# Optimization experiments

Hardware: AMD Instinct MI355X
Metric: run time of the kernel (lower is better)

## Reference

```python
import jax, jax.numpy as jnp
import numpy as np

K_BINS, EMB_WIDTH = 2048, 64
N, T = 8, 8192

def setup_inputs() -> dict:
    key = jax.random.key(0)
    k1, k2 = jax.random.split(key)
    x = jax.random.normal(k1, (N, EMB_WIDTH, T), dtype=jnp.float32)
    mask = jnp.ones((N, 1, T), dtype=jnp.float32)
    k = jax.random.normal(k2, (K_BINS, EMB_WIDTH), dtype=jnp.float32)
    return {"x": x, "mask": mask, "k": k}

def reference(x, mask, k):
    # Faithful forward of BottleneckBlock.forward with update_k=False and
    # codebook `k` already initialized (init path is a stateful randperm init).
    n, c, t = x.shape
    w = k.shape[1]
    # preprocess: [N, W, T] -> [N*T, W]
    xf = jnp.transpose(x, (0, 2, 1)).reshape(-1, c)
    mf = jnp.transpose(mask, (0, 2, 1)).reshape(-1, 1)
    prenorm = jnp.linalg.norm(xf - jnp.mean(xf)) / np.sqrt(float(xf.size))
    dist = (jnp.sum(xf * xf, axis=-1, keepdims=True)
            - 2.0 * (xf @ k.T)
            + jnp.sum(k * k, axis=-1)[None, :])  # [N*T, k_bins]
    x_l = jnp.argmin(dist, axis=-1)              # [N*T]
    fit = jax.lax.stop_gradient(jnp.mean(jnp.min(dist, axis=-1)))
    x_d = jax.lax.stop_gradient(k[x_l])          # dequantize, no_grad in torch
    # commit loss: mask is 0/1, so masked-row norm^2 == sum(mask * diff^2)
    diff2 = jnp.sum((x_d - xf) ** 2, axis=-1, keepdims=True)
    commit_loss = jnp.sum(mf * diff2) / (jnp.sum(mf) * w)
    # straight-through estimator + mask
    x_d = (xf + jax.lax.stop_gradient(x_d - xf)) * mf
    # postprocess: back to [N, W, T] and [N, T]
    x_d = jnp.transpose(x_d.reshape(n, t, w), (0, 2, 1))
    x_l = x_l.reshape(n, t)
    return x_l, x_d, commit_loss, fit, prenorm
```

## Files before the change

kernel.cpp:

```cpp
#include <hip/hip_runtime.h>

#define T_DIM 8192
#define N_DIM 8
#define C_DIM 64
#define KB    2048
#define NT    (N_DIM * T_DIM)
#define TOTX  ((size_t)NT * C_DIM)
#define NBLK  2048
#define LISTCAP 65536
#define TAU   0.04f

#define SCR_COUNT 0
#define SCR_LIST  16
#define SCR_PART  65792
#define SCR_KK    82432
#define SCR_K     90112
#define SCR_FIX   262144

typedef _Float16 half_t;
typedef _Float16 f16x8 __attribute__((ext_vector_type(8)));
typedef float    f32x16 __attribute__((ext_vector_type(16)));

__device__ __forceinline__ float np_sumsq64(const float* __restrict__ a) {
    float r[8];
    #pragma unroll
    for (int j = 0; j < 8; ++j) r[j] = __fmul_rn(a[j], a[j]);
    #pragma unroll
    for (int i = 8; i < 64; i += 8)
        #pragma unroll
        for (int j = 0; j < 8; ++j)
            r[j] = __fadd_rn(r[j], __fmul_rn(a[i + j], a[i + j]));
    return __fadd_rn(__fadd_rn(__fadd_rn(r[0], r[1]), __fadd_rn(r[2], r[3])),
                     __fadd_rn(__fadd_rn(r[4], r[5]), __fadd_rn(r[6], r[7])));
}

__global__ __launch_bounds__(64) void kprep_kernel(const float* __restrict__ k,
                                                   float* __restrict__ out) {
    float* base = out + NT;
    const int bin = blockIdx.x * 64 + threadIdx.x;
    if (bin == 0) ((int*)base)[SCR_COUNT] = 0;

    float kv[64];
    #pragma unroll
    for (int i = 0; i < 16; ++i)
        *(float4*)&kv[i * 4] = *(const float4*)(k + (size_t)bin * 64 + i * 4);

    float kn = 0.f;
    #pragma unroll
    for (int c = 0; c < 64; ++c) kn = fmaf(kv[c], kv[c], kn);
    base[SCR_KK + bin] = np_sumsq64(kv);

    f16x8* kscr = (f16x8*)(base + SCR_K);
    const int ch = bin >> 7, b127 = bin & 127;
    #pragma unroll
    for (int slot = 0; slot < 8; ++slot) {
        f16x8 h8;
        #pragma unroll
        for (int e = 0; e < 8; ++e)
            h8[e] = (half_t)(-2.f * (float)((half_t)kv[slot * 8 + e]));
        kscr[(size_t)ch * 1152 + slot * 128 + b127] = h8;
    }
    {
        half_t knh = (half_t)kn;
        half_t knl = (half_t)(kn - (float)knh);
        f16x8 k8;
        #pragma unroll
        for (int e = 0; e < 8; ++e) k8[e] = (half_t)0.f;
        k8[0] = knh; k8[1] = knl;
        kscr[(size_t)ch * 1152 + 1024 + b127] = k8;
    }
}

__global__ __launch_bounds__(256, 2) void argmin_kernel(const float* __restrict__ x,
                                                        const float* __restrict__ mask,
                                                        float* __restrict__ out) {
    __shared__ __align__(16) f16x8 xhi_s[256];
    __shared__ float psx[8][32], psxx[8][32];
    __shared__ float wres[4][32][3];

    float* base = out + NT;
    const int tid = threadIdx.x;
    const int l   = tid & 63, w = tid >> 6;
    const int col = l & 31, kg = l >> 5;
    const int r0  = blockIdx.x * 32;
    const int n   = r0 >> 13;
    const int t0  = r0 & (T_DIM - 1);

    {
        const int row = tid & 31, slot = tid >> 5;
        float sx = 0.f, sxx = 0.f;
        f16x8 h8;
        #pragma unroll
        for (int e = 0; e < 8; ++e) {
            float v = x[((size_t)n * C_DIM + slot * 8 + e) * T_DIM + t0 + row];
            h8[e] = (half_t)v;
            sx += v; sxx = fmaf(v, v, sxx);
        }
        xhi_s[slot * 32 + row] = h8;
        psx[slot][row]  = sx;
        psxx[slot][row] = sxx;
    }
    __syncthreads();

    f16x8 a0 = xhi_s[(0 + kg) * 32 + col];
    f16x8 a1 = xhi_s[(2 + kg) * 32 + col];
    f16x8 a2 = xhi_s[(4 + kg) * 32 + col];
    f16x8 a3 = xhi_s[(6 + kg) * 32 + col];
    f16x8 aones;
    #pragma unroll
    for (int e = 0; e < 8; ++e) aones[e] = (half_t)0.f;
    if (kg == 0) { aones[0] = (half_t)1.f; aones[1] = (half_t)1.f; }

    const f16x8* kf0 = (const f16x8*)(base + SCR_K) + (size_t)w * 4 * 1152 + col;
    const int kgo = kg * 128;

    f32x16 zacc;
    #pragma unroll
    for (int r = 0; r < 16; ++r) zacc[r] = 0.f;

    float bv0 = __builtin_inff(), b20 = __builtin_inff(); int c0 = 0;
    float bv1 = __builtin_inff(), b21 = __builtin_inff(); int c1 = 0;
    float bv2 = __builtin_inff(), b22 = __builtin_inff(); int c2 = 0;
    float bv3 = __builtin_inff(), b23 = __builtin_inff(); int c3 = 0;

    f16x8 bA[4], bB[4], b4A, b4B;

#define LOADT(t, BH, B4)                                            \
    {                                                               \
        const f16x8* p = kf0 + (((t) >> 2) * 1152 + ((t) & 3) * 32);\
        BH[0] = p[kgo]; BH[1] = p[kgo + 256];                       \
        BH[2] = p[kgo + 512]; BH[3] = p[kgo + 768];                 \
        B4 = p[1024];                                               \
    }

#define UPD(J, RR, CODE)                                                     \
    {                                                                        \
        float sv = acc[RR];                                                  \
        float nb2;                                                           \
        asm("v_med3_f32 %0, %1, %2, %3"                                      \
            : "=v"(nb2) : "v"(sv), "v"(bv##J), "v"(b2##J));                  \
        b2##J = nb2;                                                         \
        if (sv < bv##J) { bv##J = sv; c##J = (CODE); }                       \
    }

#define COMPT(t, BH, B4)                                                     \
    {                                                                        \
        f32x16 acc = __builtin_amdgcn_mfma_f32_32x32x16_f16(B4, aones, zacc, 0, 0, 0); \
        acc = __builtin_amdgcn_mfma_f32_32x32x16_f16(BH[0], a0, acc, 0, 0, 0); \
        acc = __builtin_amdgcn_mfma_f32_32x32x16_f16(BH[1], a1, acc, 0, 0, 0); \
        acc = __builtin_amdgcn_mfma_f32_32x32x16_f16(BH[2], a2, acc, 0, 0, 0); \
        acc = __builtin_amdgcn_mfma_f32_32x32x16_f16(BH[3], a3, acc, 0, 0, 0); \
        const int cb = w * 512 + (t) * 32;                                   \
        UPD(0, 0, cb + 0)  UPD(0, 1, cb + 1)  UPD(0, 2, cb + 2)  UPD(0, 3, cb + 3) \
        UPD(1, 4, cb + 8)  UPD(1, 5, cb + 9)  UPD(1, 6, cb + 10) UPD(1, 7, cb + 11) \
        UPD(2, 8, cb + 16) UPD(2, 9, cb + 17) UPD(2, 10, cb + 18) UPD(2, 11, cb + 19) \
        UPD(3, 12, cb + 24) UPD(3, 13, cb + 25) UPD(3, 14, cb + 26) UPD(3, 15, cb + 27) \
    }

    LOADT(0, bA, b4A);
    #pragma unroll 1
    for (int t = 0; t < 14; t += 2) {
        LOADT(t + 1, bB, b4B);
        COMPT(t, bA, b4A);
        LOADT(t + 2, bA, b4A);
        COMPT(t + 1, bB, b4B);
    }
    LOADT(15, bB, b4B);
    COMPT(14, bA, b4A);
    COMPT(15, bB, b4B);
#undef LOADT
#undef COMPT
#undef UPD

    const int hi4 = kg * 4;
    c0 += hi4; c1 += hi4; c2 += hi4; c3 += hi4;

    float bv, b2; int bb;
    {
        float m01v; int m01c; float m01s;
        if (bv1 < bv0 || (bv1 == bv0 && c1 < c0)) { m01v = bv1; m01c = c1; }
        else                                      { m01v = bv0; m01c = c0; }
        m01s = fminf(fminf(b20, b21), fmaxf(bv0, bv1));
        float m23v; int m23c; float m23s;
        if (bv3 < bv2 || (bv3 == bv2 && c3 < c2)) { m23v = bv3; m23c = c3; }
        else                                      { m23v = bv2; m23c = c2; }
        m23s = fminf(fminf(b22, b23), fmaxf(bv2, bv3));
        if (m23v < m01v || (m23v == m01v && m23c < m01c)) { bv = m23v; bb = m23c; }
        else                                              { bv = m01v; bb = m01c; }
        b2 = fminf(fminf(m01s, m23s), fmaxf(m01v, m23v));
    }

    {
        float ov = __shfl_xor(bv, 32, 64);
        float o2 = __shfl_xor(b2, 32, 64);
        int   ob = __shfl_xor(bb, 32, 64);
        b2 = fminf(fminf(b2, o2), fmaxf(bv, ov));
        if (ov < bv || (ov == bv && ob < bb)) { bv = ov; bb = ob; }
    }

    if (kg == 0) {
        wres[w][col][0] = bv;
        wres[w][col][1] = b2;
        wres[w][col][2] = __int_as_float(bb);
    }
    __syncthreads();

    if (tid < 32) {
        const int row = tid;
        const float v0 = wres[0][row][0], v1 = wres[1][row][0];
        const float v2 = wres[2][row][0], v3 = wres[3][row][0];
        float fbv = v0; int fbb = __float_as_int(wres[0][row][2]);
        if (v1 < fbv) { fbv = v1; fbb = __float_as_int(wres[1][row][2]); }
        if (v2 < fbv) { fbv = v2; fbb = __float_as_int(wres[2][row][2]); }
        if (v3 < fbv) { fbv = v3; fbb = __float_as_int(wres[3][row][2]); }
        const float m01 = fminf(v0, v1), M01 = fmaxf(v0, v1);
        const float m23 = fminf(v2, v3), M23 = fmaxf(v2, v3);
        const float sec = fminf(fmaxf(m01, m23), fminf(M01, M23));
        const float fb2 = fminf(sec,
            fminf(fminf(wres[0][row][1], wres[1][row][1]),
                  fminf(wres[2][row][1], wres[3][row][1])));

        out[r0 + row] = (float)fbb;
        if (fb2 - fbv < TAU) {
            int idx = atomicAdd((int*)base + SCR_COUNT, 1);
            if (idx < LISTCAP) ((int*)base + SCR_LIST)[idx] = r0 + row;
        }
        float sx = 0.f, sxx = 0.f;
        #pragma unroll
        for (int sp = 0; sp < 8; ++sp) { sx += psx[sp][row]; sxx += psxx[sp][row]; }
        const float m  = mask[r0 + row];
        const float d2 = sxx + fbv;
        float vals[5] = { m * d2, d2, m, sx, sxx };
        #pragma unroll
        for (int off = 1; off <= 16; off <<= 1)
            #pragma unroll
            for (int q = 0; q < 5; ++q) vals[q] += __shfl_xor(vals[q], off, 64);
        if (tid == 0) {
            float* partials = base + SCR_PART;
            #pragma unroll
            for (int q = 0; q < 5; ++q)
                partials[(size_t)blockIdx.x * 8 + q] = vals[q];
        }
    }
}

__global__ __launch_bounds__(256) void fixup_kernel(const float* __restrict__ x,
                                                    const float* __restrict__ k,
                                                    float* __restrict__ out) {
    __shared__ float xs[32][65];
    __shared__ float sxx_s[32];
    __shared__ float redv[256];
    __shared__ int   redb[256];

    const int tid = threadIdx.x;
    float* base = out + NT;
    const int* count    = (const int*)base + SCR_COUNT;
    const int* flaglist = (const int*)base + SCR_LIST;
    const float* kk     = base + SCR_KK;
    float* fix          = base + SCR_FIX;
    int cnt = *count;
    if (cnt > LISTCAP) cnt = LISTCAP;
    const int nb8 = ((cnt + 31) >> 5) << 3;

    const int rloc = tid & 31, part = tid >> 5;

    for (int wk = blockIdx.x; wk < nb8; wk += gridDim.x) {
        const int bi = wk >> 3, chunk = wk & 7;
        int li = bi * 32 + rloc;
        if (li >= cnt) li = bi * 32;
        const int row = flaglist[li];
        const int n = row >> 13, t = row & (T_DIM - 1);
        #pragma unroll
        for (int e = 0; e < 8; ++e)
            xs[rloc][part * 8 + e] = x[((size_t)n * C_DIM + part * 8 + e) * T_DIM + t];
        __syncthreads();
        if (tid < 32) sxx_s[tid] = np_sumsq64(&xs[tid][0]);
        __syncthreads();

        float xr[64];
        #pragma unroll
        for (int c = 0; c < 64; ++c) xr[c] = xs[rloc][c];
        const float xx = sxx_s[rloc];

        float bv = __builtin_inff();
        int   bb = 0x7fffffff;
        const int bbase = chunk * 256 + part * 32;
        #pragma unroll 1
        for (int i = 0; i < 32; i += 2) {
            const int b0 = bbase + i;
            const int b1 = b0 + 1;
            const float* k0 = k + (size_t)b0 * 64;
            const float* k1 = k + (size_t)b1 * 64;
            float d0 = 0.f, d1 = 0.f;
            #pragma unroll
            for (int c = 0; c < 64; ++c) {
                d0 = fmaf(xr[c], k0[c], d0);
                d1 = fmaf(xr[c], k1[c], d1);
            }
            float s0 = __fadd_rn(__fsub_rn(xx, __fadd_rn(d0, d0)), kk[b0]);
            float s1 = __fadd_rn(__fsub_rn(xx, __fadd_rn(d1, d1)), kk[b1]);
            if (s0 < bv || (s0 == bv && b0 < bb)) { bv = s0; bb = b0; }
            if (s1 < bv || (s1 == bv && b1 < bb)) { bv = s1; bb = b1; }
        }
        redv[tid] = bv; redb[tid] = bb;
        __syncthreads();
        if (tid < 32) {
            float fv = redv[tid]; int fb = redb[tid];
            #pragma unroll
            for (int p = 1; p < 8; ++p) {
                float ov = redv[p * 32 + tid];
                int   ob = redb[p * 32 + tid];
                if (ov < fv || (ov == fv && ob < fb)) { fv = ov; fb = ob; }
            }
            const int fi = bi * 32 + tid;
            if (fi < cnt) {
                fix[(size_t)fi * 16 + chunk * 2]     = fv;
                fix[(size_t)fi * 16 + chunk * 2 + 1] = __int_as_float(fb);
            }
        }
        __syncthreads();
    }
}

__global__ __launch_bounds__(256) void fixmerge_kernel(float* __restrict__ out) {
    float* base = out + NT;
    const int* count    = (const int*)base + SCR_COUNT;
    const int* flaglist = (const int*)base + SCR_LIST;
    const float* fix    = base + SCR_FIX;
    const int tid = threadIdx.x;
    int cnt = *count;
    if (cnt > LISTCAP) cnt = LISTCAP;

    for (int fi = blockIdx.x * 256 + tid; fi < cnt; fi += gridDim.x * 256) {
        const float* p = fix + (size_t)fi * 16;
        float bv = p[0];
        int   bb = __float_as_int(p[1]);
        #pragma unroll
        for (int c = 1; c < 8; ++c) {
            float v = p[c * 2];
            int   b = __float_as_int(p[c * 2 + 1]);
            if (v < bv || (v == bv && b < bb)) { bv = v; bb = b; }
        }
        out[flaglist[fi]] = (float)bb;
    }

    if (blockIdx.x == 0) {
        const float* partials = base + SCR_PART;
        double vals[5] = {0, 0, 0, 0, 0};
        for (int i = tid; i < NBLK; i += 256)
            #pragma unroll
            for (int q = 0; q < 5; ++q) vals[q] += (double)partials[(size_t)i * 8 + q];
        #pragma unroll
        for (int off = 1; off <= 32; off <<= 1)
            #pragma unroll
            for (int q = 0; q < 5; ++q) vals[q] += __shfl_xor(vals[q], off, 64);
        __shared__ double sred[4][5];
        const int wid = tid >> 6, lane = tid & 63;
        if (lane == 0)
            for (int q = 0; q < 5; ++q) sred[wid][q] = vals[q];
        __syncthreads();
        if (tid == 0) {
            double cm  = sred[0][0] + sred[1][0] + sred[2][0] + sred[3][0];
            double fs  = sred[0][1] + sred[1][1] + sred[2][1] + sred[3][1];
            double ms  = sred[0][2] + sred[1][2] + sred[2][2] + sred[3][2];
            double sx  = sred[0][3] + sred[1][3] + sred[2][3] + sred[3][3];
            double sxx = sred[0][4] + sred[1][4] + sred[2][4] + sred[3][4];
            double sz  = (double)TOTX;
            out[NT + TOTX + 0] = (float)(cm / (ms * (double)C_DIM));
            out[NT + TOTX + 1] = (float)(fs / (double)NT);
            out[NT + TOTX + 2] = (float)sqrt(fmax(0.0, (sxx - sx * sx / sz) / sz));
        }
    }
}

__global__ __launch_bounds__(256) void xd_kernel(const float* __restrict__ mask,
                                                 const float* __restrict__ k,
                                                 float* __restrict__ out) {
    const int row = blockIdx.x * 256 + threadIdx.x;
    const int n = row >> 13, t = row & (T_DIM - 1);
    const int b = (int)out[row];
    const float m = mask[row];
    const float* kr = k + (size_t)b * C_DIM;
    float* xd = out + NT;
    #pragma unroll
    for (int c = 0; c < C_DIM; ++c)
        xd[((size_t)n * C_DIM + c) * T_DIM + t] = kr[c] * m;
}

extern "C" void kernel_launch(void* const* d_in, const int* in_sizes, int n_in,
                              void* d_out, int out_size, void* d_ws, size_t ws_size,
                              hipStream_t stream) {
    (void)in_sizes; (void)n_in; (void)out_size; (void)d_ws; (void)ws_size;
    const float* x    = (const float*)d_in[0];
    const float* mask = (const float*)d_in[1];
    const float* k    = (const float*)d_in[2];
    float* out = (float*)d_out;

    kprep_kernel<<<32, 64, 0, stream>>>(k, out);
    argmin_kernel<<<NBLK, 256, 0, stream>>>(x, mask, out);
    fixup_kernel<<<2048, 256, 0, stream>>>(x, k, out);
    fixmerge_kernel<<<256, 256, 0, stream>>>(out);
    xd_kernel<<<NT / 256, 256, 0, stream>>>(mask, k, out);
}
```

Before: 79.51 us.

## Pack bin index into distance low bits and fuse dequantize write into argmin

The argmin inner loop now stores a 6-bit local code in the low mantissa bits of each distance, so the running best becomes a plain fminf with no separate index tracking. Scratch moves to the workspace buffer when it is large enough, which lets argmin write x_d directly for its rows and lets fixmerge rewrite x_d for corrected rows. This removes the separate xd kernel launch and the re-read of indices. TAU is widened slightly to cover the precision lost to the truncated mantissa, which may flag more rows for the exact fixup pass.

```diff
diff --git a/kernel.cpp b/kernel.cpp
--- a/kernel.cpp
+++ b/kernel.cpp
@@ -8,7 +8,7 @@
 #define TOTX  ((size_t)NT * C_DIM)
 #define NBLK  2048
 #define LISTCAP 65536
-#define TAU   0.04f
+#define TAU   0.045f
 
 #define SCR_COUNT 0
 #define SCR_LIST  16
@@ -16,6 +16,7 @@
 #define SCR_KK    82432
 #define SCR_K     90112
 #define SCR_FIX   262144
+#define WS_NEED_BYTES ((size_t)1310720 * 4)
 
 typedef _Float16 half_t;
 typedef _Float16 f16x8 __attribute__((ext_vector_type(8)));
@@ -35,8 +36,7 @@
 }
 
 __global__ __launch_bounds__(64) void kprep_kernel(const float* __restrict__ k,
-                                                   float* __restrict__ out) {
-    float* base = out + NT;
+                                                   float* __restrict__ base) {
     const int bin = blockIdx.x * 64 + threadIdx.x;
     if (bin == 0) ((int*)base)[SCR_COUNT] = 0;
 
@@ -71,14 +71,17 @@
     }
 }
 
+template <int WSMODE>
 __global__ __launch_bounds__(256, 2) void argmin_kernel(const float* __restrict__ x,
                                                         const float* __restrict__ mask,
-                                                        float* __restrict__ out) {
+                                                        const float* __restrict__ k,
+                                                        float* __restrict__ out,
+                                                        float* __restrict__ base) {
     __shared__ __align__(16) f16x8 xhi_s[256];
     __shared__ float psx[8][32], psxx[8][32];
     __shared__ float wres[4][32][3];
-
-    float* base = out + NT;
+    __shared__ int   sbest_s[32];
+
     const int tid = threadIdx.x;
     const int l   = tid & 63, w = tid >> 6;
     const int col = l & 31, kg = l >> 5;
@@ -118,10 +121,10 @@
     #pragma unroll
     for (int r = 0; r < 16; ++r) zacc[r] = 0.f;
 
-    float bv0 = __builtin_inff(), b20 = __builtin_inff(); int c0 = 0;
-    float bv1 = __builtin_inff(), b21 = __builtin_inff(); int c1 = 0;
-    float bv2 = __builtin_inff(), b22 = __builtin_inff(); int c2 = 0;
-    float bv3 = __builtin_inff(), b23 = __builtin_inff(); int c3 = 0;
+    float bv0 = __builtin_inff(), b20 = __builtin_inff();
+    float bv1 = __builtin_inff(), b21 = __builtin_inff();
+    float bv2 = __builtin_inff(), b22 = __builtin_inff();
+    float bv3 = __builtin_inff(), b23 = __builtin_inff();
 
     f16x8 bA[4], bB[4], b4A, b4B;
 
@@ -135,12 +138,13 @@
 
 #define UPD(J, RR, CODE)                                                     \
     {                                                                        \
-        float sv = acc[RR];                                                  \
+        float spf = __uint_as_float(                                         \
+            (__float_as_uint(acc[RR]) & 0xFFFFFFC0u) | (unsigned)(CODE));    \
         float nb2;                                                           \
         asm("v_med3_f32 %0, %1, %2, %3"                                      \
-            : "=v"(nb2) : "v"(sv), "v"(bv##J), "v"(b2##J));                  \
+            : "=v"(nb2) : "v"(spf), "v"(bv##J), "v"(b2##J));                 \
         b2##J = nb2;                                                         \
-        if (sv < bv##J) { bv##J = sv; c##J = (CODE); }                       \
+        bv##J = fminf(bv##J, spf);                                           \
     }
 
 #define COMPT(t, BH, B4)                                                     \
@@ -150,11 +154,11 @@
         acc = __builtin_amdgcn_mfma_f32_32x32x16_f16(BH[1], a1, acc, 0, 0, 0); \
         acc = __builtin_amdgcn_mfma_f32_32x32x16_f16(BH[2], a2, acc, 0, 0, 0); \
         acc = __builtin_amdgcn_mfma_f32_32x32x16_f16(BH[3], a3, acc, 0, 0, 0); \
-        const int cb = w * 512 + (t) * 32;                                   \
-        UPD(0, 0, cb + 0)  UPD(0, 1, cb + 1)  UPD(0, 2, cb + 2)  UPD(0, 3, cb + 3) \
-        UPD(1, 4, cb + 8)  UPD(1, 5, cb + 9)  UPD(1, 6, cb + 10) UPD(1, 7, cb + 11) \
-        UPD(2, 8, cb + 16) UPD(2, 9, cb + 17) UPD(2, 10, cb + 18) UPD(2, 11, cb + 19) \
-        UPD(3, 12, cb + 24) UPD(3, 13, cb + 25) UPD(3, 14, cb + 26) UPD(3, 15, cb + 27) \
+        const int cb4 = (t) * 4;                                             \
+        UPD(0, 0, cb4 + 0)  UPD(0, 1, cb4 + 1)  UPD(0, 2, cb4 + 2)  UPD(0, 3, cb4 + 3) \
+        UPD(1, 4, cb4 + 0)  UPD(1, 5, cb4 + 1)  UPD(1, 6, cb4 + 2)  UPD(1, 7, cb4 + 3) \
+        UPD(2, 8, cb4 + 0)  UPD(2, 9, cb4 + 1)  UPD(2, 10, cb4 + 2) UPD(2, 11, cb4 + 3) \
+        UPD(3, 12, cb4 + 0) UPD(3, 13, cb4 + 1) UPD(3, 14, cb4 + 2) UPD(3, 15, cb4 + 3) \
     }
 
     LOADT(0, bA, b4A);
@@ -172,8 +176,15 @@
 #undef COMPT
 #undef UPD
 
-    const int hi4 = kg * 4;
-    c0 += hi4; c1 += hi4; c2 += hi4; c3 += hi4;
+    const int bbase = w * 512 + 4 * kg;
+    int c0, c1, c2, c3;
+    {
+        unsigned q;
+        q = __float_as_uint(bv0) & 63u; c0 = bbase + (int)(q >> 2) * 32 + 0  + (int)(q & 3);
+        q = __float_as_uint(bv1) & 63u; c1 = bbase + (int)(q >> 2) * 32 + 8  + (int)(q & 3);
+        q = __float_as_uint(bv2) & 63u; c2 = bbase + (int)(q >> 2) * 32 + 16 + (int)(q & 3);
+        q = __float_as_uint(bv3) & 63u; c3 = bbase + (int)(q >> 2) * 32 + 24 + (int)(q & 3);
+    }
 
     float bv, b2; int bb;
     {
@@ -221,6 +232,7 @@
                   fminf(wres[2][row][1], wres[3][row][1])));
 
         out[r0 + row] = (float)fbb;
+        sbest_s[row] = fbb;
         if (fb2 - fbv < TAU) {
             int idx = atomicAdd((int*)base + SCR_COUNT, 1);
             if (idx < LISTCAP) ((int*)base + SCR_LIST)[idx] = r0 + row;
@@ -242,18 +254,29 @@
                 partials[(size_t)blockIdx.x * 8 + q] = vals[q];
         }
     }
+
+    if (WSMODE) {
+        __syncthreads();
+        const int row = tid & 31, slot = tid >> 5;
+        const int b = sbest_s[row];
+        const float m = mask[r0 + row];
+        float* xd = out + NT;
+        #pragma unroll
+        for (int e = 0; e < 8; ++e)
+            xd[((size_t)n * C_DIM + slot * 8 + e) * T_DIM + t0 + row] =
+                k[(size_t)b * C_DIM + slot * 8 + e] * m;
+    }
 }
 
 __global__ __launch_bounds__(256) void fixup_kernel(const float* __restrict__ x,
                                                     const float* __restrict__ k,
-                                                    float* __restrict__ out) {
+                                                    float* __restrict__ base) {
     __shared__ float xs[32][65];
     __shared__ float sxx_s[32];
     __shared__ float redv[256];
     __shared__ int   redb[256];
 
     const int tid = threadIdx.x;
-    float* base = out + NT;
     const int* count    = (const int*)base + SCR_COUNT;
     const int* flaglist = (const int*)base + SCR_LIST;
     const float* kk     = base + SCR_KK;
@@ -322,8 +345,11 @@
     }
 }
 
-__global__ __launch_bounds__(256) void fixmerge_kernel(float* __restrict__ out) {
-    float* base = out + NT;
+template <int WSMODE>
+__global__ __launch_bounds__(256) void fixmerge_kernel(const float* __restrict__ mask,
+                                                       const float* __restrict__ k,
+                                                       float* __restrict__ out,
+                                                       float* __restrict__ base) {
     const int* count    = (const int*)base + SCR_COUNT;
     const int* flaglist = (const int*)base + SCR_LIST;
     const float* fix    = base + SCR_FIX;
@@ -341,7 +367,17 @@
             int   b = __float_as_int(p[c * 2 + 1]);
             if (v < bv || (v == bv && b < bb)) { bv = v; bb = b; }
         }
-        out[flaglist[fi]] = (float)bb;
+        const int row = flaglist[fi];
+        out[row] = (float)bb;
+        if (WSMODE) {
+            const int n = row >> 13, t = row & (T_DIM - 1);
+            const float m = mask[row];
+            const float* kr = k + (size_t)bb * C_DIM;
+            float* xd = out + NT;
+            #pragma unroll
+            for (int c = 0; c < C_DIM; ++c)
+                xd[((size_t)n * C_DIM + c) * T_DIM + t] = kr[c] * m;
+        }
     }
 
     if (blockIdx.x == 0) {
@@ -390,15 +426,24 @@
 extern "C" void kernel_launch(void* const* d_in, const int* in_sizes, int n_in,
                               void* d_out, int out_size, void* d_ws, size_t ws_size,
                               hipStream_t stream) {
-    (void)in_sizes; (void)n_in; (void)out_size; (void)d_ws; (void)ws_size;
+    (void)in_sizes; (void)n_in; (void)out_size;
     const float* x    = (const float*)d_in[0];
     const float* mask = (const float*)d_in[1];
     const float* k    = (const float*)d_in[2];
     float* out = (float*)d_out;
 
-    kprep_kernel<<<32, 64, 0, stream>>>(k, out);
-    argmin_kernel<<<NBLK, 256, 0, stream>>>(x, mask, out);
-    fixup_kernel<<<2048, 256, 0, stream>>>(x, k, out);
-    fixmerge_kernel<<<256, 256, 0, stream>>>(out);
-    xd_kernel<<<NT / 256, 256, 0, stream>>>(mask, k, out);
-}
+    if (ws_size >= WS_NEED_BYTES) {
+        float* base = (float*)d_ws;
+        kprep_kernel<<<32, 64, 0, stream>>>(k, base);
+        argmin_kernel<1><<<NBLK, 256, 0, stream>>>(x, mask, k, out, base);
+        fixup_kernel<<<2048, 256, 0, stream>>>(x, k, base);
+        fixmerge_kernel<1><<<256, 256, 0, stream>>>(mask, k, out, base);
+    } else {
+        float* base = out + NT;
+        kprep_kernel<<<32, 64, 0, stream>>>(k, base);
+        argmin_kernel<0><<<NBLK, 256, 0, stream>>>(x, mask, k, out, base);
+        fixup_kernel<<<2048, 256, 0, stream>>>(x, k, base);
+        fixmerge_kernel<0><<<256, 256, 0, stream>>>(mask, k, out, base);
+        xd_kernel<<<NT / 256, 256, 0, stream>>>(mask, k, out);
+    }
+}
```

New measurement: 92.64 us. +16.5%, slower.
